# Kernel tuning notes

Hardware: AMD Instinct MI355X
Metric: run time of the kernel (lower is better)

Reference implementation:

```python
import jax, jax.numpy as jnp
import numpy as np

B, N, E = 64, 256, 512   # batch, leaves (power of 2), embed_size
D, U = 512, 512          # tree_size, units (controller size == units)


def setup_inputs() -> dict:
    key = jax.random.key(0)
    ks = jax.random.split(key, 11)
    sc = lambda k, shape: jax.random.normal(k, shape, dtype=jnp.float32) * 0.05
    return {
        "inputs": jax.random.normal(ks[0], (B, N, E), dtype=jnp.float32),
        "h0": sc(ks[1], (B, U)),
        "c0": sc(ks[2], (B, U)),
        "W_t": sc(ks[3], (E, D)),          # Transformer
        "W_j": sc(ks[4], (2 * D, D)),      # Join
        "W_s": sc(ks[5], (D + U, 1)),      # Search
        "W_h": sc(ks[6], (D + U, D)),      # Write candidate
        "W_T": sc(ks[7], (D + U, 1)),      # Write gate
        "kernel": sc(ks[8], (E, 4 * U)),   # LSTM input kernel (i,f,c,o)
        "rec_kernel": sc(ks[9], (U, 4 * U)),
        "bias": jnp.zeros((4 * U,), jnp.float32),
    }


def reference(inputs, h0, c0, W_t, W_j, W_s, W_h, W_T, kernel, rec_kernel, bias):
    b, n, e = inputs.shape
    control = h0  # control = previous LSTM hidden state

    # --- leaf embed: Transformer, batched over all leaves ---
    leaf_h = jax.nn.relu(jnp.einsum('bne,ed->bnd', inputs, W_t))  # [B,N,D]

    # --- refresh: bottom-up join, batched per tree level ---
    levels = [leaf_h]
    h = leaf_h
    while h.shape[1] > 1:
        pair = jnp.concatenate([h[:, 0::2], h[:, 1::2]], axis=-1)  # [B,m/2,2D]
        h = jax.nn.relu(jnp.einsum('bmk,kd->bmd', pair, W_j))
        levels.append(h)

    # --- retrieve: top-down search producing leaf attentions ---
    # Searches all use refresh-time h (parent search happens before any
    # update in its subtree), so a level-batched top-down pass is exact.
    attn = jnp.ones((b, 1, 1), inputs.dtype)
    for lvl in range(len(levels) - 1, 0, -1):
        node_h = levels[lvl]                     # [B,m,D]
        m = node_h.shape[1]
        ctrl = jnp.broadcast_to(control[:, None, :], (b, m, control.shape[-1]))
        mr = jax.nn.sigmoid(jnp.einsum('bmk,ko->bmo',
                                       jnp.concatenate([node_h, ctrl], -1), W_s))  # [B,m,1]
        # children interleave: left gets attn*(1-mr), right gets attn*mr
        attn = jnp.concatenate([attn * (1.0 - mr), attn * mr], axis=-1).reshape(b, 2 * m, 1)

    tree_out = jnp.sum(attn * inputs, axis=1)  # [B,E] soft-retrieved leaf value

    # --- write update of leaf memories, batched over all leaves ---
    ctrl = jnp.broadcast_to(control[:, None, :], (b, n, control.shape[-1]))
    data = jnp.concatenate([leaf_h, ctrl], -1)                     # [B,N,D+U]
    cand = jax.nn.sigmoid(jnp.einsum('bnk,kd->bnd', data, W_h))
    upd = jax.nn.sigmoid(jnp.einsum('bnk,ko->bno', data, W_T))
    written = upd * cand + (1.0 - upd) * leaf_h
    leaf_h_new = attn * written + (1.0 - attn) * leaf_h            # [B,N,D]

    # --- LSTM cell update (keras LSTMCell gate order i,f,c,o) ---
    z = tree_out @ kernel + h0 @ rec_kernel + bias
    zi, zf, zg, zo = jnp.split(z, 4, axis=-1)
    c_new = jax.nn.sigmoid(zf) * c0 + jax.nn.sigmoid(zi) * jnp.tanh(zg)
    h_new = jax.nn.sigmoid(zo) * jnp.tanh(c_new)
    return h_new, c_new, leaf_h_new
```

## Files before the change

### kernel.cpp

```cpp
#include <hip/hip_runtime.h>
#include <hip/hip_bf16.h>
#include <cstdint>
#include <cstddef>


__device__ __forceinline__ float sigmoidf_(float x) { return 1.0f / (1.0f + __expf(-x)); }

typedef __attribute__((ext_vector_type(8))) short bf16x8;
typedef __attribute__((ext_vector_type(4))) float f32x4;

__device__ __forceinline__ void load_lds16(const void* g, void* l) {
  __builtin_amdgcn_global_load_lds((const __attribute__((address_space(1))) void*)g,
                                   (__attribute__((address_space(3))) void*)l, 16, 0, 0);
}

__global__ __launch_bounds__(256)
void cvt_inputs(const float* __restrict__ in, __hip_bfloat16* __restrict__ outp) {
  const size_t i = ((size_t)blockIdx.x * 256 + threadIdx.x) * 8;
  float4 v0 = *(const float4*)(in + i);
  float4 v1 = *(const float4*)(in + i + 4);
  union { __hip_bfloat16 h[8]; bf16x8 v; } u;
  u.h[0] = __float2bfloat16(v0.x); u.h[1] = __float2bfloat16(v0.y);
  u.h[2] = __float2bfloat16(v0.z); u.h[3] = __float2bfloat16(v0.w);
  u.h[4] = __float2bfloat16(v1.x); u.h[5] = __float2bfloat16(v1.y);
  u.h[6] = __float2bfloat16(v1.z); u.h[7] = __float2bfloat16(v1.w);
  *(bf16x8*)(outp + i) = u.v;
}

__global__ __launch_bounds__(256)
void tconv_all(const float* __restrict__ W_t, const float* __restrict__ W_j,
               const float* __restrict__ W_h,
               __hip_bfloat16* __restrict__ Wt_t, __hip_bfloat16* __restrict__ Wt_j,
               __hip_bfloat16* __restrict__ Wt_h) {
  const int z = blockIdx.z;
  if (z != 1 && blockIdx.x >= 16) return;
  const int K = (z == 1) ? 1024 : 512;
  const float* W = (z == 0) ? W_t : ((z == 1) ? W_j : W_h);
  __hip_bfloat16* Wt = (z == 0) ? Wt_t : ((z == 1) ? Wt_j : Wt_h);
  __shared__ float sh[32][33];
  const int tx = threadIdx.x & 31, ty = threadIdx.x >> 5;
  const int k0 = blockIdx.x * 32, n0 = blockIdx.y * 32;
#pragma unroll
  for (int i = 0; i < 4; ++i)
    sh[ty + i * 8][tx] = W[(size_t)(k0 + ty + i * 8) * 512 + n0 + tx];
  __syncthreads();
#pragma unroll
  for (int i = 0; i < 4; ++i)
    Wt[(size_t)(n0 + ty + i * 8) * K + k0 + tx] = __float2bfloat16(sh[tx][ty + i * 8]);
}

template<int MODE, bool AFP32>
__global__ __launch_bounds__(256)
void mfma_gemm(const __hip_bfloat16* __restrict__ A, const float* __restrict__ Af,
               const __hip_bfloat16* __restrict__ Bt, int M, int K,
               __hip_bfloat16* __restrict__ Cb, float* __restrict__ Cf,
               const float* __restrict__ ctrl_h, const float* __restrict__ attn,
               const float* __restrict__ upd_raw, const __hip_bfloat16* __restrict__ leaf,
               const float* __restrict__ W_T, const float* __restrict__ ctrlT) {
  __shared__ __align__(16) __hip_bfloat16 Asm[2][128 * 32];
  __shared__ __align__(16) __hip_bfloat16 Bsm[2][128 * 32];
  const int tid = threadIdx.x;
  const int wave = tid >> 6, lane = tid & 63;
  const int bm = blockIdx.x * 128, bn = blockIdx.y * 128;
  const int wm = (wave >> 1) * 64, wn = (wave & 1) * 64;
  const int q = lane >> 4, lr = lane & 15;

  f32x4 acc[4][4] = {};

  const int c0 = wave * 128 + lane, c1 = c0 + 64;
  const size_t ga0 = (size_t)(bm + (c0 >> 2)) * K + (c0 & 3) * 8;
  const size_t ga1 = (size_t)(bm + (c1 >> 2)) * K + (c1 & 3) * 8;
  const size_t gb0 = (size_t)(bn + (c0 >> 2)) * K + (c0 & 3) * 8;
  const size_t gb1 = (size_t)(bn + (c1 >> 2)) * K + (c1 & 3) * 8;

  if constexpr (AFP32) {
    for (int k0v = 0; k0v < K; k0v += 32) {
#pragma unroll
      for (int it = 0; it < 4; ++it) {
        const int c = it * 256 + tid;
        const int row = c >> 3, kc = c & 7;
        float4 v = *(const float4*)(Af + (size_t)(bm + row) * K + k0v + kc * 4);
        __hip_bfloat16 h[4] = {__float2bfloat16(v.x), __float2bfloat16(v.y),
                               __float2bfloat16(v.z), __float2bfloat16(v.w)};
        *(ushort4*)(Asm[0] + row * 32 + kc * 4) = *(ushort4*)h;
      }
      load_lds16(Bt + gb0 + k0v, Bsm[0] + wave * 1024);
      load_lds16(Bt + gb1 + k0v, Bsm[0] + wave * 1024 + 512);
      __syncthreads();
      bf16x8 af[4], bfr[4];
#pragma unroll
      for (int mt = 0; mt < 4; ++mt)
        af[mt] = *(const bf16x8*)(Asm[0] + (wm + mt * 16 + lr) * 32 + q * 8);
#pragma unroll
      for (int nt = 0; nt < 4; ++nt)
        bfr[nt] = *(const bf16x8*)(Bsm[0] + (wn + nt * 16 + lr) * 32 + q * 8);
#pragma unroll
      for (int mt = 0; mt < 4; ++mt)
#pragma unroll
        for (int nt = 0; nt < 4; ++nt)
          acc[mt][nt] = __builtin_amdgcn_mfma_f32_16x16x32_bf16(af[mt], bfr[nt], acc[mt][nt], 0, 0, 0);
      __syncthreads();
    }
  } else {
    auto stage = [&](int s, int kv) {
      load_lds16(A + ga0 + kv, Asm[s] + wave * 1024);
      load_lds16(A + ga1 + kv, Asm[s] + wave * 1024 + 512);
      load_lds16(Bt + gb0 + kv, Bsm[s] + wave * 1024);
      load_lds16(Bt + gb1 + kv, Bsm[s] + wave * 1024 + 512);
    };
    stage(0, 0);
    __syncthreads();
    int cur = 0;
    for (int kv = 0; kv < K; kv += 32) {
      if (kv + 32 < K) stage(cur ^ 1, kv + 32);
      bf16x8 af[4], bfr[4];
#pragma unroll
      for (int mt = 0; mt < 4; ++mt)
        af[mt] = *(const bf16x8*)(Asm[cur] + (wm + mt * 16 + lr) * 32 + q * 8);
#pragma unroll
      for (int nt = 0; nt < 4; ++nt)
        bfr[nt] = *(const bf16x8*)(Bsm[cur] + (wn + nt * 16 + lr) * 32 + q * 8);
#pragma unroll
      for (int mt = 0; mt < 4; ++mt)
#pragma unroll
        for (int nt = 0; nt < 4; ++nt)
          acc[mt][nt] = __builtin_amdgcn_mfma_f32_16x16x32_bf16(af[mt], bfr[nt], acc[mt][nt], 0, 0, 0);
      __syncthreads();
      cur ^= 1;
    }
  }

  if (MODE == 0) {
#pragma unroll
    for (int mt = 0; mt < 4; ++mt) {
      const int rbase = bm + wm + mt * 16 + q * 4;
#pragma unroll
      for (int nt = 0; nt < 4; ++nt) {
        const int col = bn + wn + nt * 16 + lr;
#pragma unroll
        for (int r = 0; r < 4; ++r) {
          const int row = rbase + r;
          if (row < M)
            Cb[(size_t)row * 512 + col] = __float2bfloat16(fmaxf(acc[mt][nt][r], 0.f));
        }
      }
    }
    if (upd_raw) {
      float wt[4];
#pragma unroll
      for (int nt = 0; nt < 4; ++nt) wt[nt] = W_T[bn + wn + nt * 16 + lr];
#pragma unroll
      for (int mt = 0; mt < 4; ++mt) {
        const int rbase = bm + wm + mt * 16 + q * 4;
#pragma unroll
        for (int r = 0; r < 4; ++r) {
          float p = 0.f;
#pragma unroll
          for (int nt = 0; nt < 4; ++nt) {
            const float v = __bfloat162float(__float2bfloat16(fmaxf(acc[mt][nt][r], 0.f)));
            p += v * wt[nt];
          }
          p += __shfl_xor(p, 1); p += __shfl_xor(p, 2);
          p += __shfl_xor(p, 4); p += __shfl_xor(p, 8);
          if (lr == 0) atomicAdd((float*)&upd_raw[rbase + r], p);
        }
      }
    }
  } else {
#pragma unroll
    for (int mt = 0; mt < 4; ++mt) {
      const int rbase = bm + wm + mt * 16 + q * 4;
#pragma unroll
      for (int r = 0; r < 4; ++r) {
        const int row = rbase + r;
        const float a = attn[row];
        const int bidx = row >> 8;
        const float u = sigmoidf_(upd_raw[row] + ctrlT[bidx]);
#pragma unroll
        for (int nt = 0; nt < 4; ++nt) {
          const int col = bn + wn + nt * 16 + lr;
          const float cand = sigmoidf_(acc[mt][nt][r] + ctrl_h[(size_t)bidx * 512 + col]);
          const float lf = __bfloat162float(leaf[(size_t)row * 512 + col]);
          const float w = u * cand + (1.f - u) * lf;
          Cf[(size_t)row * 512 + col] = a * w + (1.f - a) * lf;
        }
      }
    }
  }
}

__global__ __launch_bounds__(256)
void join_level(const __hip_bfloat16* __restrict__ in, __hip_bfloat16* __restrict__ outp,
                const __hip_bfloat16* __restrict__ Wt_j) {
  const int wave = threadIdx.x >> 6, lane = threadIdx.x & 63;
  const int q = lane >> 4, lr = lane & 15;
  const int tile = blockIdx.x * 4 + wave;
  const int mtile = tile >> 5, ntile = tile & 31;
  const __hip_bfloat16* ap = in + (size_t)(mtile * 16 + lr) * 1024 + q * 8;
  const __hip_bfloat16* bp = Wt_j + (size_t)(ntile * 16 + lr) * 1024 + q * 8;
  f32x4 acc = {0.f, 0.f, 0.f, 0.f};
#pragma unroll 8
  for (int k0 = 0; k0 < 1024; k0 += 32) {
    bf16x8 a  = *(const bf16x8*)(ap + k0);
    bf16x8 bb = *(const bf16x8*)(bp + k0);
    acc = __builtin_amdgcn_mfma_f32_16x16x32_bf16(a, bb, acc, 0, 0, 0);
  }
  const int col = ntile * 16 + lr;
  const int orow = mtile * 16 + q * 4;
#pragma unroll
  for (int r = 0; r < 4; ++r)
    outp[(size_t)(orow + r) * 512 + col] = __float2bfloat16(fmaxf(acc[r], 0.f));
}

__global__ __launch_bounds__(256)
void ctrl_prep(const float* __restrict__ h0, const float* __restrict__ W_h,
               const float* __restrict__ W_T, float* __restrict__ ch,
               float* __restrict__ ctrlT) {
  const int b = blockIdx.y, tid = threadIdx.x;
  if (blockIdx.x == 2) {
    __shared__ float part[256];
    float p = 0.f;
    for (int i = tid; i < 512; i += 256) p += h0[b * 512 + i] * W_T[512 + i];
    part[tid] = p; __syncthreads();
    for (int s = 128; s > 0; s >>= 1) { if (tid < s) part[tid] += part[tid + s]; __syncthreads(); }
    if (tid == 0) ctrlT[b] = part[0];
  } else {
    __shared__ float hsh[512];
    hsh[tid]       = h0[b * 512 + tid];
    hsh[tid + 256] = h0[b * 512 + 256 + tid];
    __syncthreads();
    const int col = blockIdx.x * 256 + tid;
    const float* Wp = W_h + (size_t)512 * 512 + col;
    float s = 0.f;
#pragma unroll 8
    for (int k = 0; k < 512; ++k) s += hsh[k] * Wp[(size_t)k * 512];
    ch[(size_t)b * 512 + col] = s;
  }
}

__global__ __launch_bounds__(256)
void propagate_sc(const __hip_bfloat16* __restrict__ levels, const float* __restrict__ h0,
                  const float* __restrict__ W_s, float* __restrict__ attn_out) {
  const int b = blockIdx.x, tid = threadIdx.x;
  const int wave = tid >> 6, lane = tid & 63;
  __shared__ float part[256], ws[512], sc_sh[256], attn_sh[256], newattn[256];
  __shared__ float scs_sh;
  ws[tid] = W_s[tid]; ws[tid + 256] = W_s[tid + 256];
  float p = 0.f;
  for (int i = tid; i < 512; i += 256) p += h0[b * 512 + i] * W_s[512 + i];
  part[tid] = p; __syncthreads();
  for (int s = 128; s > 0; s >>= 1) { if (tid < s) part[tid] += part[tid + s]; __syncthreads(); }
  if (tid == 0) { scs_sh = part[0]; attn_sh[0] = 1.f; }
  __syncthreads();
  const float scs = scs_sh;
  const int rowbase[9] = {0, 0, 8192, 12288, 14336, 15360, 15872, 16128, 16256};
  const int nodeoff[9] = {0, 0, 128, 192, 224, 240, 248, 252, 254};
  for (int l = 1; l <= 8; ++l) {
    const int m = 256 >> l;
    for (int j0 = wave * 8; j0 < m; j0 += 32) {
      const int j = j0 + (lane >> 3), s = lane & 7;
      float q = 0.f;
      if (j < m) {
        const __hip_bfloat16* xr = levels + (size_t)(rowbase[l] + b * m + j) * 512;
#pragma unroll
        for (int i = 0; i < 8; ++i) {
          const int k = (i * 8 + s) * 8;
          union { bf16x8 v; __hip_bfloat16 e[8]; } u;
          u.v = *(const bf16x8*)(xr + k);
#pragma unroll
          for (int jj = 0; jj < 8; ++jj) q += __bfloat162float(u.e[jj]) * ws[k + jj];
        }
      }
      q += __shfl_xor(q, 1); q += __shfl_xor(q, 2); q += __shfl_xor(q, 4);
      if (s == 0 && j < m) sc_sh[nodeoff[l] + j] = q;
    }
  }
  __syncthreads();
#pragma unroll
  for (int l = 8; l >= 1; --l) {
    const int m = 256 >> l;
    if (tid < m) {
      const float mr = sigmoidf_(sc_sh[nodeoff[l] + tid] + scs);
      const float a = attn_sh[tid];
      newattn[2 * tid]     = a * (1.f - mr);
      newattn[2 * tid + 1] = a * mr;
    }
    __syncthreads();
    if (tid < 2 * m) attn_sh[tid] = newattn[tid];
    __syncthreads();
  }
  attn_out[b * 256 + tid] = attn_sh[tid];
}

__global__ __launch_bounds__(256)
void tree_part(const float* __restrict__ inputs, const float* __restrict__ attn,
               float* __restrict__ tp) {
  const int s = blockIdx.x, b = blockIdx.y;
  const int tid = threadIdx.x;
  __shared__ float a_sh[64];
  if (tid < 64) a_sh[tid] = attn[b * 256 + s * 64 + tid];
  __syncthreads();
  float acc0 = 0.f, acc1 = 0.f;
  const float* base = inputs + ((size_t)b * 256 + s * 64) * 512;
  for (int nn = 0; nn < 64; ++nn) {
    const float a = a_sh[nn];
    const float* row = base + (size_t)nn * 512;
    acc0 += a * row[tid];
    acc1 += a * row[tid + 256];
  }
  tp[((size_t)s * 64 + b) * 512 + tid]       = acc0;
  tp[((size_t)s * 64 + b) * 512 + tid + 256] = acc1;
}

__global__ __launch_bounds__(256)
void lstm_gemm_splitk(const float* __restrict__ tp, const float* __restrict__ h0,
                      const float* __restrict__ kern, const float* __restrict__ rec,
                      float* __restrict__ Zp) {
  const int tid = threadIdx.x;
  const int col = blockIdx.x * 256 + tid;
  const int b0 = blockIdx.y * 4;
  const int z = blockIdx.z;
  const float* W = (z < 4) ? (kern + (size_t)z * 128 * 2048)
                           : (rec + (size_t)(z - 4) * 128 * 2048);
  const int koff = (z & 3) * 128;
  __shared__ float xs[4][128];
  for (int i = tid; i < 512; i += 256) {
    int bb = i >> 7, k = i & 127;
    const size_t idx = (size_t)(b0 + bb) * 512 + koff + k;
    float x;
    if (z < 4) x = tp[idx] + tp[32768 + idx] + tp[65536 + idx] + tp[98304 + idx];
    else       x = h0[idx];
    xs[bb][k] = x;
  }
  __syncthreads();
  float a0 = 0.f, a1 = 0.f, a2 = 0.f, a3 = 0.f;
#pragma unroll 8
  for (int k = 0; k < 128; ++k) {
    const float w = W[(size_t)k * 2048 + col];
    a0 += xs[0][k] * w;
    a1 += xs[1][k] * w;
    a2 += xs[2][k] * w;
    a3 += xs[3][k] * w;
  }
  Zp[((size_t)z * 64 + b0 + 0) * 2048 + col] = a0;
  Zp[((size_t)z * 64 + b0 + 1) * 2048 + col] = a1;
  Zp[((size_t)z * 64 + b0 + 2) * 2048 + col] = a2;
  Zp[((size_t)z * 64 + b0 + 3) * 2048 + col] = a3;
}

__global__ __launch_bounds__(256)
void lstm_combine(const float* __restrict__ Zp, const float* __restrict__ bias,
                  const float* __restrict__ c0,
                  float* __restrict__ out_h, float* __restrict__ out_c) {
  const int i = blockIdx.x * 256 + threadIdx.x;
  const int b = i >> 9, u = i & 511;
  float zi = bias[u], zf = bias[512 + u], zg = bias[1024 + u], zo = bias[1536 + u];
#pragma unroll
  for (int z = 0; z < 8; ++z) {
    const size_t base = ((size_t)z * 64 + b) * 2048;
    zi += Zp[base + u];
    zf += Zp[base + 512 + u];
    zg += Zp[base + 1024 + u];
    zo += Zp[base + 1536 + u];
  }
  const float c = sigmoidf_(zf) * c0[i] + sigmoidf_(zi) * tanhf(zg);
  out_h[i] = sigmoidf_(zo) * tanhf(c);
  out_c[i] = c;
}

extern "C" void kernel_launch(void* const* d_in, const int* in_sizes, int n_in,
                              void* d_out, int out_size, void* d_ws, size_t ws_size,
                              hipStream_t stream) {
  const float* inputs = (const float*)d_in[0];
  const float* h0     = (const float*)d_in[1];
  const float* c0     = (const float*)d_in[2];
  const float* W_t    = (const float*)d_in[3];
  const float* W_j    = (const float*)d_in[4];
  const float* W_s    = (const float*)d_in[5];
  const float* W_h    = (const float*)d_in[6];
  const float* W_T    = (const float*)d_in[7];
  const float* kern   = (const float*)d_in[8];
  const float* rec    = (const float*)d_in[9];
  const float* bias   = (const float*)d_in[10];
  float* out = (float*)d_out;

  char* p = (char*)d_ws;
  __hip_bfloat16* leaf_bf   = (__hip_bfloat16*)p; p += 16777216;
  __hip_bfloat16* levels_bf = (__hip_bfloat16*)p; p += 16842752;
  __hip_bfloat16* Wt_t      = (__hip_bfloat16*)p; p += 524288;
  __hip_bfloat16* Wt_j      = (__hip_bfloat16*)p; p += 1048576;
  __hip_bfloat16* Wt_h      = (__hip_bfloat16*)p; p += 524288;
  float* attn  = (float*)p; p += 65536;
  float* upd   = (float*)p; p += 65536;
  float* ch    = (float*)p; p += 131072;
  float* ctrlT = (float*)p; p += 4096;
  float* tp    = (float*)p; p += 524288;
  float* Zp    = (float*)p; p += 4194304;
  const bool use_cvt = ws_size >= (size_t)(p - (char*)d_ws) + 16777216;
  __hip_bfloat16* inputs_bf = (__hip_bfloat16*)p;

  tconv_all<<<dim3(32, 16, 3), 256, 0, stream>>>(W_t, W_j, W_h, Wt_t, Wt_j, Wt_h);
  ctrl_prep<<<dim3(3, 64), 256, 0, stream>>>(h0, W_h, W_T, ch, ctrlT);
  hipMemsetAsync(upd, 0, 16384 * sizeof(float), stream);

  if (use_cvt) {
    cvt_inputs<<<4096, 256, 0, stream>>>(inputs, inputs_bf);
    mfma_gemm<0, false><<<dim3(128, 4), 256, 0, stream>>>(
        inputs_bf, nullptr, Wt_t, 16384, 512,
        leaf_bf, nullptr, nullptr, nullptr, upd, nullptr, W_T, nullptr);
  } else {
    mfma_gemm<0, true><<<dim3(128, 4), 256, 0, stream>>>(
        nullptr, inputs, Wt_t, 16384, 512,
        leaf_bf, nullptr, nullptr, nullptr, upd, nullptr, W_T, nullptr);
  }

  const int lvl_off_h[9] = {0, 0, 4194304, 6291456, 7340032,
                            7864320, 8126464, 8257536, 8323072};
  const __hip_bfloat16* Aptr = leaf_bf;
  for (int l = 1; l <= 3; ++l) {
    const int M = 64 * (256 >> l);
    __hip_bfloat16* Cl = levels_bf + lvl_off_h[l];
    mfma_gemm<0, false><<<dim3(M / 128, 4), 256, 0, stream>>>(
        Aptr, nullptr, Wt_j, M, 1024,
        Cl, nullptr, nullptr, nullptr, nullptr, nullptr, nullptr, nullptr);
    Aptr = Cl;
  }
  for (int l = 4; l <= 8; ++l) {
    const int m_out = 256 >> l;
    join_level<<<32 * m_out, 256, 0, stream>>>(levels_bf + lvl_off_h[l - 1],
                                               levels_bf + lvl_off_h[l], Wt_j);
  }

  propagate_sc<<<64, 256, 0, stream>>>(levels_bf, h0, W_s, attn);

  tree_part<<<dim3(4, 64), 256, 0, stream>>>(inputs, attn, tp);

  mfma_gemm<1, false><<<dim3(128, 4), 256, 0, stream>>>(
      leaf_bf, nullptr, Wt_h, 16384, 512,
      nullptr, out + 65536, ch, attn, upd, leaf_bf, nullptr, ctrlT);

  lstm_gemm_splitk<<<dim3(8, 16, 8), 256, 0, stream>>>(tp, h0, kern, rec, Zp);
  lstm_combine<<<128, 256, 0, stream>>>(Zp, bias, c0, out, out + 32768);
}
```

Measured before the change: 334.4 us.

## Fuse small kernels into merged prep, cooperative tail, and write+LSTM launches

Merges the input conversion, weight transposes, control precompute and memset into one prep kernel. The small join levels, the search propagation and the tree_part reduction move into one cooperative kernel that uses grid syncs between phases. The write-update GEMM and the LSTM split-K GEMM now run as disjoint block ranges of a single launch. The goal is to cut launch count and let independent work share the GPU, at the cost of grid-wide barriers and a large block-range dispatch inside each merged kernel.

```diff
diff --git a/kernel.cpp b/kernel.cpp
--- a/kernel.cpp
+++ b/kernel.cpp
@@ -1,8 +1,11 @@
 #include <hip/hip_runtime.h>
+#include <hip/hip_cooperative_groups.h>
 #include <hip/hip_bf16.h>
 #include <cstdint>
 #include <cstddef>
 
+namespace cg = cooperative_groups;
+
 
 __device__ __forceinline__ float sigmoidf_(float x) { return 1.0f / (1.0f + __expf(-x)); }
 
@@ -14,39 +17,73 @@
                                    (__attribute__((address_space(3))) void*)l, 16, 0, 0);
 }
 
+template<bool DO_CVT>
 __global__ __launch_bounds__(256)
-void cvt_inputs(const float* __restrict__ in, __hip_bfloat16* __restrict__ outp) {
-  const size_t i = ((size_t)blockIdx.x * 256 + threadIdx.x) * 8;
-  float4 v0 = *(const float4*)(in + i);
-  float4 v1 = *(const float4*)(in + i + 4);
-  union { __hip_bfloat16 h[8]; bf16x8 v; } u;
-  u.h[0] = __float2bfloat16(v0.x); u.h[1] = __float2bfloat16(v0.y);
-  u.h[2] = __float2bfloat16(v0.z); u.h[3] = __float2bfloat16(v0.w);
-  u.h[4] = __float2bfloat16(v1.x); u.h[5] = __float2bfloat16(v1.y);
-  u.h[6] = __float2bfloat16(v1.z); u.h[7] = __float2bfloat16(v1.w);
-  *(bf16x8*)(outp + i) = u.v;
-}
-
-__global__ __launch_bounds__(256)
-void tconv_all(const float* __restrict__ W_t, const float* __restrict__ W_j,
-               const float* __restrict__ W_h,
-               __hip_bfloat16* __restrict__ Wt_t, __hip_bfloat16* __restrict__ Wt_j,
-               __hip_bfloat16* __restrict__ Wt_h) {
-  const int z = blockIdx.z;
-  if (z != 1 && blockIdx.x >= 16) return;
-  const int K = (z == 1) ? 1024 : 512;
-  const float* W = (z == 0) ? W_t : ((z == 1) ? W_j : W_h);
-  __hip_bfloat16* Wt = (z == 0) ? Wt_t : ((z == 1) ? Wt_j : Wt_h);
-  __shared__ float sh[32][33];
-  const int tx = threadIdx.x & 31, ty = threadIdx.x >> 5;
-  const int k0 = blockIdx.x * 32, n0 = blockIdx.y * 32;
-#pragma unroll
-  for (int i = 0; i < 4; ++i)
-    sh[ty + i * 8][tx] = W[(size_t)(k0 + ty + i * 8) * 512 + n0 + tx];
-  __syncthreads();
-#pragma unroll
-  for (int i = 0; i < 4; ++i)
-    Wt[(size_t)(n0 + ty + i * 8) * K + k0 + tx] = __float2bfloat16(sh[tx][ty + i * 8]);
+void prep_all(const float* __restrict__ inputs, const float* __restrict__ W_t,
+              const float* __restrict__ W_j, const float* __restrict__ W_h,
+              const float* __restrict__ W_T, const float* __restrict__ h0,
+              __hip_bfloat16* __restrict__ inputs_bf, __hip_bfloat16* __restrict__ Wt_t,
+              __hip_bfloat16* __restrict__ Wt_j, __hip_bfloat16* __restrict__ Wt_h,
+              float* __restrict__ ch, float* __restrict__ ctrlT, float* __restrict__ upd) {
+  const int NC = DO_CVT ? 4096 : 0;
+  const int bid = blockIdx.x, tid = threadIdx.x;
+  __shared__ float shf[1056];
+  if (DO_CVT && bid < NC) {
+    const size_t i = ((size_t)bid * 256 + tid) * 8;
+    float4 v0 = *(const float4*)(inputs + i);
+    float4 v1 = *(const float4*)(inputs + i + 4);
+    union { __hip_bfloat16 h[8]; bf16x8 v; } u;
+    u.h[0] = __float2bfloat16(v0.x); u.h[1] = __float2bfloat16(v0.y);
+    u.h[2] = __float2bfloat16(v0.z); u.h[3] = __float2bfloat16(v0.w);
+    u.h[4] = __float2bfloat16(v1.x); u.h[5] = __float2bfloat16(v1.y);
+    u.h[6] = __float2bfloat16(v1.z); u.h[7] = __float2bfloat16(v1.w);
+    *(bf16x8*)(inputs_bf + i) = u.v;
+  } else if (bid < NC + 1024) {
+    const int t = bid - NC;
+    int z, bx, by;
+    if (t < 512)      { z = 1; bx = t & 31;         by = t >> 5; }
+    else if (t < 768) { z = 0; bx = (t - 512) & 15; by = (t - 512) >> 4; }
+    else              { z = 2; bx = (t - 768) & 15; by = (t - 768) >> 4; }
+    const int K = (z == 1) ? 1024 : 512;
+    const float* W = (z == 0) ? W_t : ((z == 1) ? W_j : W_h);
+    __hip_bfloat16* Wt = (z == 0) ? Wt_t : ((z == 1) ? Wt_j : Wt_h);
+    float (*sh)[33] = (float(*)[33])shf;
+    const int tx = tid & 31, ty = tid >> 5;
+    const int k0 = bx * 32, n0 = by * 32;
+#pragma unroll
+    for (int i = 0; i < 4; ++i)
+      sh[ty + i * 8][tx] = W[(size_t)(k0 + ty + i * 8) * 512 + n0 + tx];
+    __syncthreads();
+#pragma unroll
+    for (int i = 0; i < 4; ++i)
+      Wt[(size_t)(n0 + ty + i * 8) * K + k0 + tx] = __float2bfloat16(sh[tx][ty + i * 8]);
+  } else if (bid < NC + 1024 + 192) {
+    const int u = bid - NC - 1024;
+    if (u < 128) {
+      const int b = u >> 1;
+      float* hsh = shf;
+      hsh[tid]       = h0[b * 512 + tid];
+      hsh[tid + 256] = h0[b * 512 + 256 + tid];
+      __syncthreads();
+      const int col = (u & 1) * 256 + tid;
+      const float* Wp = W_h + (size_t)512 * 512 + col;
+      float s = 0.f;
+#pragma unroll 8
+      for (int k = 0; k < 512; ++k) s += hsh[k] * Wp[(size_t)k * 512];
+      ch[(size_t)b * 512 + col] = s;
+    } else {
+      const int b = u - 128;
+      float* part = shf;
+      float p = 0.f;
+      for (int i = tid; i < 512; i += 256) p += h0[b * 512 + i] * W_T[512 + i];
+      part[tid] = p; __syncthreads();
+      for (int s = 128; s > 0; s >>= 1) { if (tid < s) part[tid] += part[tid + s]; __syncthreads(); }
+      if (tid == 0) ctrlT[b] = part[0];
+    }
+  } else {
+    const int u = bid - NC - 1024 - 192;
+    *(float4*)(upd + ((size_t)u * 256 + tid) * 4) = float4{0.f, 0.f, 0.f, 0.f};
+  }
 }
 
 template<int MODE, bool AFP32>
@@ -130,43 +167,201 @@
     }
   }
 
-  if (MODE == 0) {
+#pragma unroll
+  for (int mt = 0; mt < 4; ++mt) {
+    const int rbase = bm + wm + mt * 16 + q * 4;
+#pragma unroll
+    for (int nt = 0; nt < 4; ++nt) {
+      const int col = bn + wn + nt * 16 + lr;
+#pragma unroll
+      for (int r = 0; r < 4; ++r) {
+        const int row = rbase + r;
+        if (row < M)
+          Cb[(size_t)row * 512 + col] = __float2bfloat16(fmaxf(acc[mt][nt][r], 0.f));
+      }
+    }
+  }
+  if (upd_raw) {
+    float wt[4];
+#pragma unroll
+    for (int nt = 0; nt < 4; ++nt) wt[nt] = W_T[bn + wn + nt * 16 + lr];
 #pragma unroll
     for (int mt = 0; mt < 4; ++mt) {
       const int rbase = bm + wm + mt * 16 + q * 4;
 #pragma unroll
-      for (int nt = 0; nt < 4; ++nt) {
-        const int col = bn + wn + nt * 16 + lr;
-#pragma unroll
-        for (int r = 0; r < 4; ++r) {
-          const int row = rbase + r;
-          if (row < M)
-            Cb[(size_t)row * 512 + col] = __float2bfloat16(fmaxf(acc[mt][nt][r], 0.f));
+      for (int r = 0; r < 4; ++r) {
+        float p = 0.f;
+#pragma unroll
+        for (int nt = 0; nt < 4; ++nt) {
+          const float v = __bfloat162float(__float2bfloat16(fmaxf(acc[mt][nt][r], 0.f)));
+          p += v * wt[nt];
         }
-      }
-    }
-    if (upd_raw) {
-      float wt[4];
-#pragma unroll
-      for (int nt = 0; nt < 4; ++nt) wt[nt] = W_T[bn + wn + nt * 16 + lr];
-#pragma unroll
-      for (int mt = 0; mt < 4; ++mt) {
-        const int rbase = bm + wm + mt * 16 + q * 4;
-#pragma unroll
-        for (int r = 0; r < 4; ++r) {
-          float p = 0.f;
-#pragma unroll
-          for (int nt = 0; nt < 4; ++nt) {
-            const float v = __bfloat162float(__float2bfloat16(fmaxf(acc[mt][nt][r], 0.f)));
-            p += v * wt[nt];
+        p += __shfl_xor(p, 1); p += __shfl_xor(p, 2);
+        p += __shfl_xor(p, 4); p += __shfl_xor(p, 8);
+        if (lr == 0) atomicAdd((float*)&upd_raw[rbase + r], p);
+      }
+    }
+  }
+}
+
+__global__ __launch_bounds__(256, 2)
+void tail_coop(__hip_bfloat16* __restrict__ levels, const __hip_bfloat16* __restrict__ Wt_j,
+               const float* __restrict__ h0, const float* __restrict__ W_s,
+               const float* __restrict__ inputs, float* __restrict__ attn_out,
+               float* __restrict__ tp) {
+  cg::grid_group grid = cg::this_grid();
+  const int bid = blockIdx.x, tid = threadIdx.x;
+  const int wave = tid >> 6, lane = tid & 63;
+  const int q = lane >> 4, lr = lane & 15;
+  __shared__ float part[256], ws[512], sc_sh[256], attn_sh[256], newattn[256];
+  __shared__ float scs_sh;
+  const int lvl_off[9] = {0, 0, 4194304, 6291456, 7340032,
+                          7864320, 8126464, 8257536, 8323072};
+
+  for (int l = 4; l <= 8; ++l) {
+    const int m_out = 256 >> l;
+    if (bid < 32 * m_out) {
+      const __hip_bfloat16* in = levels + lvl_off[l - 1];
+      __hip_bfloat16* outp = levels + lvl_off[l];
+      const int tile = bid * 4 + wave;
+      const int mtile = tile >> 5, ntile = tile & 31;
+      const __hip_bfloat16* ap = in + (size_t)(mtile * 16 + lr) * 1024 + q * 8;
+      const __hip_bfloat16* bp = Wt_j + (size_t)(ntile * 16 + lr) * 1024 + q * 8;
+      f32x4 acc = {0.f, 0.f, 0.f, 0.f};
+#pragma unroll 8
+      for (int k0 = 0; k0 < 1024; k0 += 32) {
+        bf16x8 a  = *(const bf16x8*)(ap + k0);
+        bf16x8 bb = *(const bf16x8*)(bp + k0);
+        acc = __builtin_amdgcn_mfma_f32_16x16x32_bf16(a, bb, acc, 0, 0, 0);
+      }
+      const int col = ntile * 16 + lr;
+      const int orow = mtile * 16 + q * 4;
+#pragma unroll
+      for (int r = 0; r < 4; ++r)
+        outp[(size_t)(orow + r) * 512 + col] = __float2bfloat16(fmaxf(acc[r], 0.f));
+    }
+    __threadfence();
+    grid.sync();
+  }
+
+  if (bid < 64) {
+    const int b = bid;
+    ws[tid] = W_s[tid]; ws[tid + 256] = W_s[tid + 256];
+    float p = 0.f;
+    for (int i = tid; i < 512; i += 256) p += h0[b * 512 + i] * W_s[512 + i];
+    part[tid] = p; __syncthreads();
+    for (int s = 128; s > 0; s >>= 1) { if (tid < s) part[tid] += part[tid + s]; __syncthreads(); }
+    if (tid == 0) { scs_sh = part[0]; attn_sh[0] = 1.f; }
+    __syncthreads();
+    const float scs = scs_sh;
+    const int rowbase[9] = {0, 0, 8192, 12288, 14336, 15360, 15872, 16128, 16256};
+    const int nodeoff[9] = {0, 0, 128, 192, 224, 240, 248, 252, 254};
+    for (int l = 1; l <= 8; ++l) {
+      const int m = 256 >> l;
+      for (int j0 = wave * 8; j0 < m; j0 += 32) {
+        const int j = j0 + (lane >> 3), s = lane & 7;
+        float qv = 0.f;
+        if (j < m) {
+          const __hip_bfloat16* xr = levels + (size_t)(rowbase[l] + b * m + j) * 512;
+#pragma unroll
+          for (int i = 0; i < 8; ++i) {
+            const int k = (i * 8 + s) * 8;
+            union { bf16x8 v; __hip_bfloat16 e[8]; } u;
+            u.v = *(const bf16x8*)(xr + k);
+#pragma unroll
+            for (int jj = 0; jj < 8; ++jj) qv += __bfloat162float(u.e[jj]) * ws[k + jj];
           }
-          p += __shfl_xor(p, 1); p += __shfl_xor(p, 2);
-          p += __shfl_xor(p, 4); p += __shfl_xor(p, 8);
-          if (lr == 0) atomicAdd((float*)&upd_raw[rbase + r], p);
         }
-      }
-    }
-  } else {
+        qv += __shfl_xor(qv, 1); qv += __shfl_xor(qv, 2); qv += __shfl_xor(qv, 4);
+        if (s == 0 && j < m) sc_sh[nodeoff[l] + j] = qv;
+      }
+    }
+    __syncthreads();
+#pragma unroll
+    for (int l = 8; l >= 1; --l) {
+      const int m = 256 >> l;
+      if (tid < m) {
+        const float mr = sigmoidf_(sc_sh[nodeoff[l] + tid] + scs);
+        const float a = attn_sh[tid];
+        newattn[2 * tid]     = a * (1.f - mr);
+        newattn[2 * tid + 1] = a * mr;
+      }
+      __syncthreads();
+      if (tid < 2 * m) attn_sh[tid] = newattn[tid];
+      __syncthreads();
+    }
+    attn_out[b * 256 + tid] = attn_sh[tid];
+  }
+  __threadfence();
+  grid.sync();
+
+  if (bid < 256) {
+    const int s = bid >> 6, b = bid & 63;
+    if (tid < 64) part[tid] = attn_out[b * 256 + s * 64 + tid];
+    __syncthreads();
+    float acc0 = 0.f, acc1 = 0.f;
+    const float* base = inputs + ((size_t)b * 256 + s * 64) * 512;
+    for (int nn = 0; nn < 64; ++nn) {
+      const float a = part[nn];
+      const float* row = base + (size_t)nn * 512;
+      acc0 += a * row[tid];
+      acc1 += a * row[tid + 256];
+    }
+    tp[((size_t)s * 64 + b) * 512 + tid]       = acc0;
+    tp[((size_t)s * 64 + b) * 512 + tid + 256] = acc1;
+  }
+}
+
+__global__ __launch_bounds__(256)
+void write_lstm(const __hip_bfloat16* __restrict__ leaf, const __hip_bfloat16* __restrict__ Bt,
+                const float* __restrict__ ctrl_h, const float* __restrict__ attn,
+                const float* __restrict__ upd_raw, const float* __restrict__ ctrlT,
+                float* __restrict__ Cf,
+                const float* __restrict__ tp, const float* __restrict__ h0,
+                const float* __restrict__ kern, const float* __restrict__ rec,
+                float* __restrict__ Zp) {
+  __shared__ __align__(16) __hip_bfloat16 Asm[2][128 * 32];
+  __shared__ __align__(16) __hip_bfloat16 Bsm[2][128 * 32];
+  const int bid = blockIdx.x, tid = threadIdx.x;
+
+  if (bid < 512) {
+    const int K = 512;
+    const int wave = tid >> 6, lane = tid & 63;
+    const int bm = (bid & 127) * 128, bn = (bid >> 7) * 128;
+    const int wm = (wave >> 1) * 64, wn = (wave & 1) * 64;
+    const int q = lane >> 4, lr = lane & 15;
+    f32x4 acc[4][4] = {};
+    const int c0 = wave * 128 + lane, c1 = c0 + 64;
+    const size_t ga0 = (size_t)(bm + (c0 >> 2)) * K + (c0 & 3) * 8;
+    const size_t ga1 = (size_t)(bm + (c1 >> 2)) * K + (c1 & 3) * 8;
+    const size_t gb0 = (size_t)(bn + (c0 >> 2)) * K + (c0 & 3) * 8;
+    const size_t gb1 = (size_t)(bn + (c1 >> 2)) * K + (c1 & 3) * 8;
+    auto stage = [&](int s, int kv) {
+      load_lds16(leaf + ga0 + kv, Asm[s] + wave * 1024);
+      load_lds16(leaf + ga1 + kv, Asm[s] + wave * 1024 + 512);
+      load_lds16(Bt + gb0 + kv, Bsm[s] + wave * 1024);
+      load_lds16(Bt + gb1 + kv, Bsm[s] + wave * 1024 + 512);
+    };
+    stage(0, 0);
+    __syncthreads();
+    int cur = 0;
+    for (int kv = 0; kv < K; kv += 32) {
+      if (kv + 32 < K) stage(cur ^ 1, kv + 32);
+      bf16x8 af[4], bfr[4];
+#pragma unroll
+      for (int mt = 0; mt < 4; ++mt)
+        af[mt] = *(const bf16x8*)(Asm[cur] + (wm + mt * 16 + lr) * 32 + q * 8);
+#pragma unroll
+      for (int nt = 0; nt < 4; ++nt)
+        bfr[nt] = *(const bf16x8*)(Bsm[cur] + (wn + nt * 16 + lr) * 32 + q * 8);
+#pragma unroll
+      for (int mt = 0; mt < 4; ++mt)
+#pragma unroll
+        for (int nt = 0; nt < 4; ++nt)
+          acc[mt][nt] = __builtin_amdgcn_mfma_f32_16x16x32_bf16(af[mt], bfr[nt], acc[mt][nt], 0, 0, 0);
+      __syncthreads();
+      cur ^= 1;
+    }
 #pragma unroll
     for (int mt = 0; mt < 4; ++mt) {
       const int rbase = bm + wm + mt * 16 + q * 4;
@@ -186,166 +381,38 @@
         }
       }
     }
-  }
-}
-
-__global__ __launch_bounds__(256)
-void join_level(const __hip_bfloat16* __restrict__ in, __hip_bfloat16* __restrict__ outp,
-                const __hip_bfloat16* __restrict__ Wt_j) {
-  const int wave = threadIdx.x >> 6, lane = threadIdx.x & 63;
-  const int q = lane >> 4, lr = lane & 15;
-  const int tile = blockIdx.x * 4 + wave;
-  const int mtile = tile >> 5, ntile = tile & 31;
-  const __hip_bfloat16* ap = in + (size_t)(mtile * 16 + lr) * 1024 + q * 8;
-  const __hip_bfloat16* bp = Wt_j + (size_t)(ntile * 16 + lr) * 1024 + q * 8;
-  f32x4 acc = {0.f, 0.f, 0.f, 0.f};
+  } else {
+    const int u = bid - 512;
+    const int col = (u & 7) * 256 + tid;
+    const int b0 = ((u >> 3) & 15) * 4;
+    const int z = u >> 7;
+    const float* W = (z < 4) ? (kern + (size_t)z * 128 * 2048)
+                             : (rec + (size_t)(z - 4) * 128 * 2048);
+    const int koff = (z & 3) * 128;
+    float (*xs)[128] = (float(*)[128])(&Asm[0][0]);
+    for (int i = tid; i < 512; i += 256) {
+      int bb = i >> 7, k = i & 127;
+      const size_t idx = (size_t)(b0 + bb) * 512 + koff + k;
+      float x;
+      if (z < 4) x = tp[idx] + tp[32768 + idx] + tp[65536 + idx] + tp[98304 + idx];
+      else       x = h0[idx];
+      xs[bb][k] = x;
+    }
+    __syncthreads();
+    float a0 = 0.f, a1 = 0.f, a2 = 0.f, a3 = 0.f;
 #pragma unroll 8
-  for (int k0 = 0; k0 < 1024; k0 += 32) {
-    bf16x8 a  = *(const bf16x8*)(ap + k0);
-    bf16x8 bb = *(const bf16x8*)(bp + k0);
-    acc = __builtin_amdgcn_mfma_f32_16x16x32_bf16(a, bb, acc, 0, 0, 0);
-  }
-  const int col = ntile * 16 + lr;
-  const int orow = mtile * 16 + q * 4;
-#pragma unroll
-  for (int r = 0; r < 4; ++r)
-    outp[(size_t)(orow + r) * 512 + col] = __float2bfloat16(fmaxf(acc[r], 0.f));
-}
-
-__global__ __launch_bounds__(256)
-void ctrl_prep(const float* __restrict__ h0, const float* __restrict__ W_h,
-               const float* __restrict__ W_T, float* __restrict__ ch,
-               float* __restrict__ ctrlT) {
-  const int b = blockIdx.y, tid = threadIdx.x;
-  if (blockIdx.x == 2) {
-    __shared__ float part[256];
-    float p = 0.f;
-    for (int i = tid; i < 512; i += 256) p += h0[b * 512 + i] * W_T[512 + i];
-    part[tid] = p; __syncthreads();
-    for (int s = 128; s > 0; s >>= 1) { if (tid < s) part[tid] += part[tid + s]; __syncthreads(); }
-    if (tid == 0) ctrlT[b] = part[0];
-  } else {
-    __shared__ float hsh[512];
-    hsh[tid]       = h0[b * 512 + tid];
-    hsh[tid + 256] = h0[b * 512 + 256 + tid];
-    __syncthreads();
-    const int col = blockIdx.x * 256 + tid;
-    const float* Wp = W_h + (size_t)512 * 512 + col;
-    float s = 0.f;
-#pragma unroll 8
-    for (int k = 0; k < 512; ++k) s += hsh[k] * Wp[(size_t)k * 512];
-    ch[(size_t)b * 512 + col] = s;
-  }
-}
-
-__global__ __launch_bounds__(256)
-void propagate_sc(const __hip_bfloat16* __restrict__ levels, const float* __restrict__ h0,
-                  const float* __restrict__ W_s, float* __restrict__ attn_out) {
-  const int b = blockIdx.x, tid = threadIdx.x;
-  const int wave = tid >> 6, lane = tid & 63;
-  __shared__ float part[256], ws[512], sc_sh[256], attn_sh[256], newattn[256];
-  __shared__ float scs_sh;
-  ws[tid] = W_s[tid]; ws[tid + 256] = W_s[tid + 256];
-  float p = 0.f;
-  for (int i = tid; i < 512; i += 256) p += h0[b * 512 + i] * W_s[512 + i];
-  part[tid] = p; __syncthreads();
-  for (int s = 128; s > 0; s >>= 1) { if (tid < s) part[tid] += part[tid + s]; __syncthreads(); }
-  if (tid == 0) { scs_sh = part[0]; attn_sh[0] = 1.f; }
-  __syncthreads();
-  const float scs = scs_sh;
-  const int rowbase[9] = {0, 0, 8192, 12288, 14336, 15360, 15872, 16128, 16256};
-  const int nodeoff[9] = {0, 0, 128, 192, 224, 240, 248, 252, 254};
-  for (int l = 1; l <= 8; ++l) {
-    const int m = 256 >> l;
-    for (int j0 = wave * 8; j0 < m; j0 += 32) {
-      const int j = j0 + (lane >> 3), s = lane & 7;
-      float q = 0.f;
-      if (j < m) {
-        const __hip_bfloat16* xr = levels + (size_t)(rowbase[l] + b * m + j) * 512;
-#pragma unroll
-        for (int i = 0; i < 8; ++i) {
-          const int k = (i * 8 + s) * 8;
-          union { bf16x8 v; __hip_bfloat16 e[8]; } u;
-          u.v = *(const bf16x8*)(xr + k);
-#pragma unroll
-          for (int jj = 0; jj < 8; ++jj) q += __bfloat162float(u.e[jj]) * ws[k + jj];
-        }
-      }
-      q += __shfl_xor(q, 1); q += __shfl_xor(q, 2); q += __shfl_xor(q, 4);
-      if (s == 0 && j < m) sc_sh[nodeoff[l] + j] = q;
-    }
-  }
-  __syncthreads();
-#pragma unroll
-  for (int l = 8; l >= 1; --l) {
-    const int m = 256 >> l;
-    if (tid < m) {
-      const float mr = sigmoidf_(sc_sh[nodeoff[l] + tid] + scs);
-      const float a = attn_sh[tid];
-      newattn[2 * tid]     = a * (1.f - mr);
-      newattn[2 * tid + 1] = a * mr;
-    }
-    __syncthreads();
-    if (tid < 2 * m) attn_sh[tid] = newattn[tid];
-    __syncthreads();
-  }
-  attn_out[b * 256 + tid] = attn_sh[tid];
-}
-
-__global__ __launch_bounds__(256)
-void tree_part(const float* __restrict__ inputs, const float* __restrict__ attn,
-               float* __restrict__ tp) {
-  const int s = blockIdx.x, b = blockIdx.y;
-  const int tid = threadIdx.x;
-  __shared__ float a_sh[64];
-  if (tid < 64) a_sh[tid] = attn[b * 256 + s * 64 + tid];
-  __syncthreads();
-  float acc0 = 0.f, acc1 = 0.f;
-  const float* base = inputs + ((size_t)b * 256 + s * 64) * 512;
-  for (int nn = 0; nn < 64; ++nn) {
-    const float a = a_sh[nn];
-    const float* row = base + (size_t)nn * 512;
-    acc0 += a * row[tid];
-    acc1 += a * row[tid + 256];
-  }
-  tp[((size_t)s * 64 + b) * 512 + tid]       = acc0;
-  tp[((size_t)s * 64 + b) * 512 + tid + 256] = acc1;
-}
-
-__global__ __launch_bounds__(256)
-void lstm_gemm_splitk(const float* __restrict__ tp, const float* __restrict__ h0,
-                      const float* __restrict__ kern, const float* __restrict__ rec,
-                      float* __restrict__ Zp) {
-  const int tid = threadIdx.x;
-  const int col = blockIdx.x * 256 + tid;
-  const int b0 = blockIdx.y * 4;
-  const int z = blockIdx.z;
-  const float* W = (z < 4) ? (kern + (size_t)z * 128 * 2048)
-                           : (rec + (size_t)(z - 4) * 128 * 2048);
-  const int koff = (z & 3) * 128;
-  __shared__ float xs[4][128];
-  for (int i = tid; i < 512; i += 256) {
-    int bb = i >> 7, k = i & 127;
-    const size_t idx = (size_t)(b0 + bb) * 512 + koff + k;
-    float x;
-    if (z < 4) x = tp[idx] + tp[32768 + idx] + tp[65536 + idx] + tp[98304 + idx];
-    else       x = h0[idx];
-    xs[bb][k] = x;
-  }
-  __syncthreads();
-  float a0 = 0.f, a1 = 0.f, a2 = 0.f, a3 = 0.f;
-#pragma unroll 8
-  for (int k = 0; k < 128; ++k) {
-    const float w = W[(size_t)k * 2048 + col];
-    a0 += xs[0][k] * w;
-    a1 += xs[1][k] * w;
-    a2 += xs[2][k] * w;
-    a3 += xs[3][k] * w;
-  }
-  Zp[((size_t)z * 64 + b0 + 0) * 2048 + col] = a0;
-  Zp[((size_t)z * 64 + b0 + 1) * 2048 + col] = a1;
-  Zp[((size_t)z * 64 + b0 + 2) * 2048 + col] = a2;
-  Zp[((size_t)z * 64 + b0 + 3) * 2048 + col] = a3;
+    for (int k = 0; k < 128; ++k) {
+      const float w = W[(size_t)k * 2048 + col];
+      a0 += xs[0][k] * w;
+      a1 += xs[1][k] * w;
+      a2 += xs[2][k] * w;
+      a3 += xs[3][k] * w;
+    }
+    Zp[((size_t)z * 64 + b0 + 0) * 2048 + col] = a0;
+    Zp[((size_t)z * 64 + b0 + 1) * 2048 + col] = a1;
+    Zp[((size_t)z * 64 + b0 + 2) * 2048 + col] = a2;
+    Zp[((size_t)z * 64 + b0 + 3) * 2048 + col] = a3;
+  }
 }
 
 __global__ __launch_bounds__(256)
@@ -399,16 +466,15 @@
   const bool use_cvt = ws_size >= (size_t)(p - (char*)d_ws) + 16777216;
   __hip_bfloat16* inputs_bf = (__hip_bfloat16*)p;
 
-  tconv_all<<<dim3(32, 16, 3), 256, 0, stream>>>(W_t, W_j, W_h, Wt_t, Wt_j, Wt_h);
-  ctrl_prep<<<dim3(3, 64), 256, 0, stream>>>(h0, W_h, W_T, ch, ctrlT);
-  hipMemsetAsync(upd, 0, 16384 * sizeof(float), stream);
-
   if (use_cvt) {
-    cvt_inputs<<<4096, 256, 0, stream>>>(inputs, inputs_bf);
+    prep_all<true><<<4096 + 1024 + 192 + 16, 256, 0, stream>>>(
+        inputs, W_t, W_j, W_h, W_T, h0, inputs_bf, Wt_t, Wt_j, Wt_h, ch, ctrlT, upd);
     mfma_gemm<0, false><<<dim3(128, 4), 256, 0, stream>>>(
         inputs_bf, nullptr, Wt_t, 16384, 512,
         leaf_bf, nullptr, nullptr, nullptr, upd, nullptr, W_T, nullptr);
   } else {
+    prep_all<false><<<1024 + 192 + 16, 256, 0, stream>>>(
+        inputs, W_t, W_j, W_h, W_T, h0, nullptr, Wt_t, Wt_j, Wt_h, ch, ctrlT, upd);
     mfma_gemm<0, true><<<dim3(128, 4), 256, 0, stream>>>(
         nullptr, inputs, Wt_t, 16384, 512,
         leaf_bf, nullptr, nullptr, nullptr, upd, nullptr, W_T, nullptr);
@@ -425,20 +491,21 @@
         Cl, nullptr, nullptr, nullptr, nullptr, nullptr, nullptr, nullptr);
     Aptr = Cl;
   }
-  for (int l = 4; l <= 8; ++l) {
-    const int m_out = 256 >> l;
-    join_level<<<32 * m_out, 256, 0, stream>>>(levels_bf + lvl_off_h[l - 1],
-                                               levels_bf + lvl_off_h[l], Wt_j);
-  }
-
-  propagate_sc<<<64, 256, 0, stream>>>(levels_bf, h0, W_s, attn);
-
-  tree_part<<<dim3(4, 64), 256, 0, stream>>>(inputs, attn, tp);
-
-  mfma_gemm<1, false><<<dim3(128, 4), 256, 0, stream>>>(
-      leaf_bf, nullptr, Wt_h, 16384, 512,
-      nullptr, out + 65536, ch, attn, upd, leaf_bf, nullptr, ctrlT);
-
-  lstm_gemm_splitk<<<dim3(8, 16, 8), 256, 0, stream>>>(tp, h0, kern, rec, Zp);
+
+  {
+    __hip_bfloat16* lv = levels_bf;
+    const __hip_bfloat16* wj = Wt_j;
+    const float* h0p = h0;
+    const float* wsp = W_s;
+    const float* inp = inputs;
+    float* attnp = attn;
+    float* tpp = tp;
+    void* cargs[] = {&lv, &wj, &h0p, &wsp, &inp, &attnp, &tpp};
+    hipLaunchCooperativeKernel((void*)tail_coop, dim3(512), dim3(256), cargs, 0, stream);
+  }
+
+  write_lstm<<<1536, 256, 0, stream>>>(leaf_bf, Wt_h, ch, attn, upd, ctrlT,
+                                       out + 65536, tp, h0, kern, rec, Zp);
+
   lstm_combine<<<128, 256, 0, stream>>>(Zp, bias, c0, out, out + 32768);
 }
```

Measured after the change: 929.2 us. 178% more time.
